# Kernel tuning notes

Hardware: AMD Instinct MI355X
Metric: run time of the kernel (lower is better)

The kernel has to match this reference:

```python
import jax, jax.numpy as jnp
import numpy as np

N, DIN, DOUT = 8192, 256, 128
NEG_SLOPE = 0.01         # F.leaky_relu default
MASK_VAL = -9.0e15       # from the torch source


def setup_inputs() -> dict:
    key = jax.random.key(0)
    kx, kadj, kW, kbW, ka1, ka2, kba = jax.random.split(key, 7)
    x = jax.random.normal(kx, (N, DIN), dtype=jnp.float32)
    adj = jax.random.randint(kadj, (N, N), 0, 2, dtype=jnp.int32)
    # Linear W: input_dim -> output_dim
    W = jax.random.normal(kW, (DIN, DOUT), dtype=jnp.float32) * (1.0 / np.sqrt(DIN))
    bW = jax.random.normal(kbW, (DOUT,), dtype=jnp.float32) * 0.01
    # Linear a: 2*output_dim -> 1, split into the h_i part (a1) and h_j part (a2)
    a1 = jax.random.normal(ka1, (DOUT,), dtype=jnp.float32) * (1.0 / np.sqrt(2 * DOUT))
    a2 = jax.random.normal(ka2, (DOUT,), dtype=jnp.float32) * (1.0 / np.sqrt(2 * DOUT))
    ba = jax.random.normal(kba, (), dtype=jnp.float32) * 0.01
    return {"x": x, "adj": adj, "W": W, "bW": bW, "a1": a1, "a2": a2, "ba": ba}


def reference(x, adj, W, bW, a1, a2, ba):
    # h = W x + b  -> [N, DOUT]
    h = x @ W + bW
    # e[i,j] = leaky_relu(a . [h_i, h_j] + ba) = leaky_relu(a1.h_i + a2.h_j + ba)
    s_src = h @ a1            # [N]
    s_dst = h @ a2            # [N]
    e = s_src[:, None] + s_dst[None, :] + ba   # [N, N]
    e = jnp.where(e > 0, e, NEG_SLOPE * e)
    # mask non-edges, row softmax over neighbors j
    e = jnp.where(adj > 0, e, MASK_VAL)
    alpha = jax.nn.softmax(e, axis=1)          # [N, N]
    # dropout is identity in eval mode (dropout_rate=0)
    return alpha @ h                            # [N, DOUT]
```

## Files before the change

kernel.cpp:

```cpp
#include <hip/hip_runtime.h>
#include <hip/hip_bf16.h>


#define NN 8192
#define DIN 256
#define DOUT 128
#define LOG2E 1.4426950408889634f

typedef __attribute__((ext_vector_type(8))) short short8;
typedef __attribute__((ext_vector_type(4))) float floatx4;
typedef __attribute__((ext_vector_type(4))) unsigned int uintx4;

__global__ void prep_wt(const float* __restrict__ W, __hip_bfloat16* __restrict__ WT) {
    int e = blockIdx.x * blockDim.x + threadIdx.x;
    if (e < DIN * DOUT) {
        int k = e >> 7;
        int d = e & 127;
        WT[d * DIN + k] = __float2bfloat16(W[e]);
    }
}

__global__ __launch_bounds__(256, 4) void gat_h(
    const float* __restrict__ x, const __hip_bfloat16* __restrict__ WT,
    const float* __restrict__ bW, const float* __restrict__ a1, const float* __restrict__ a2,
    __hip_bfloat16* __restrict__ hbB, float* __restrict__ s_src, float* __restrict__ s_dst) {
    int tid = threadIdx.x;
    int w = tid >> 6, lane = tid & 63;
    int lm = lane & 15, lq = lane >> 4;
    int i0 = blockIdx.x * 32;
    int r0 = (w >> 1) * 16;
    int c0 = (w & 1) * 64;

    __shared__ float s1s[32], s2s[32];
    if (tid < 32) { s1s[tid] = 0.f; s2s[tid] = 0.f; }
    __syncthreads();

    floatx4 acc[4] = {};
#pragma unroll
    for (int kk = 0; kk < DIN; kk += 32) {
        const float4* xp = (const float4*)&x[(size_t)(i0 + r0 + lm) * DIN + kk + lq * 8];
        float4 xa = xp[0], xb = xp[1];
        union { short8 v; __hip_bfloat16 h[8]; } af;
        af.h[0] = __float2bfloat16(xa.x); af.h[1] = __float2bfloat16(xa.y);
        af.h[2] = __float2bfloat16(xa.z); af.h[3] = __float2bfloat16(xa.w);
        af.h[4] = __float2bfloat16(xb.x); af.h[5] = __float2bfloat16(xb.y);
        af.h[6] = __float2bfloat16(xb.z); af.h[7] = __float2bfloat16(xb.w);
#pragma unroll
        for (int t = 0; t < 4; t++) {
            int d = c0 + 16 * t + lm;
            short8 bf = *(const short8*)&WT[(size_t)d * DIN + kk + lq * 8];
            acc[t] = __builtin_amdgcn_mfma_f32_16x16x32_bf16(af.v, bf, acc[t], 0, 0, 0);
        }
    }
    float s1[4] = {0.f, 0.f, 0.f, 0.f}, s2[4] = {0.f, 0.f, 0.f, 0.f};
#pragma unroll
    for (int t = 0; t < 4; t++) {
        int d = c0 + 16 * t + lm;
        int f = (c0 >> 4) + t;
        float A1 = a1[d], A2 = a2[d], B = bW[d];
#pragma unroll
        for (int r = 0; r < 4; r++) {
            int k = r0 + lq * 4 + r;
            float h = acc[t][r] + B;
            hbB[(size_t)blockIdx.x * 4096 + f * 512 + (k >> 3) * 128 + lm * 8 + (k & 7)] =
                __float2bfloat16(h);
            s1[r] += h * A1;
            s2[r] += h * A2;
        }
    }
#pragma unroll
    for (int r = 0; r < 4; r++) {
        for (int m = 1; m < 16; m <<= 1) {
            s1[r] += __shfl_xor(s1[r], m, 64);
            s2[r] += __shfl_xor(s2[r], m, 64);
        }
    }
    if (lm == 0) {
#pragma unroll
        for (int r = 0; r < 4; r++) {
            int row = r0 + lq * 4 + r;
            atomicAdd(&s1s[row], s1[r]);
            atomicAdd(&s2s[row], s2[r]);
        }
    }
    __syncthreads();
    if (tid < 32) {
        s_src[i0 + tid] = s1s[tid] * LOG2E;
        s_dst[i0 + tid] = s2s[tid] * LOG2E;
    }
}

__device__ inline short8 make_pfrag(uintx4 m0, uintx4 m1, float ssi, float4 cd0, float4 cd1,
                                    floatx4* accd, const short8 ones) {
    float p[8];
    float e;
    e = ssi + cd0.x; e = fmaxf(e, 0.01f * e); p[0] = m0.x ? __builtin_amdgcn_exp2f(e) : 0.f;
    e = ssi + cd0.y; e = fmaxf(e, 0.01f * e); p[1] = m0.y ? __builtin_amdgcn_exp2f(e) : 0.f;
    e = ssi + cd0.z; e = fmaxf(e, 0.01f * e); p[2] = m0.z ? __builtin_amdgcn_exp2f(e) : 0.f;
    e = ssi + cd0.w; e = fmaxf(e, 0.01f * e); p[3] = m0.w ? __builtin_amdgcn_exp2f(e) : 0.f;
    e = ssi + cd1.x; e = fmaxf(e, 0.01f * e); p[4] = m1.x ? __builtin_amdgcn_exp2f(e) : 0.f;
    e = ssi + cd1.y; e = fmaxf(e, 0.01f * e); p[5] = m1.y ? __builtin_amdgcn_exp2f(e) : 0.f;
    e = ssi + cd1.z; e = fmaxf(e, 0.01f * e); p[6] = m1.z ? __builtin_amdgcn_exp2f(e) : 0.f;
    e = ssi + cd1.w; e = fmaxf(e, 0.01f * e); p[7] = m1.w ? __builtin_amdgcn_exp2f(e) : 0.f;
    union { short8 v; __hip_bfloat162 q[4]; } af;
    af.q[0] = __float22bfloat162_rn(make_float2(p[0], p[1]));
    af.q[1] = __float22bfloat162_rn(make_float2(p[2], p[3]));
    af.q[2] = __float22bfloat162_rn(make_float2(p[4], p[5]));
    af.q[3] = __float22bfloat162_rn(make_float2(p[6], p[7]));
    *accd = __builtin_amdgcn_mfma_f32_16x16x32_bf16(af.v, ones, *accd, 0, 0, 0);
    return af.v;
}

template <int NJT>
__global__ __launch_bounds__(256, 4) void gat_attn(
    const int* __restrict__ adj, const float* __restrict__ s_src,
    const float* __restrict__ s_dst, const float* __restrict__ ba_p,
    const __hip_bfloat16* __restrict__ hbB,
    float* __restrict__ num, float* __restrict__ lpart) {
    int tid = threadIdx.x;
    int w = tid >> 6, lane = tid & 63;
    int lm = lane & 15, lq = lane >> 4;
    int b = blockIdx.x;
    int ib = b & 63;
    int jh = b >> 6;
    int i0 = ib * 128 + w * 32;
    int jb0 = jh * (NJT * 32);

    const int* arow0 = adj + (size_t)(i0 + lm) * NN + jb0 + lq * 8;
    const int* arow1 = arow0 + (size_t)16 * NN;

    float ba = ba_p[0] * LOG2E;
    float ssi0 = s_src[i0 + lm] + ba;
    float ssi1 = s_src[i0 + 16 + lm] + ba;
    const float* sd = s_dst + jb0 + lq * 8;
    const __hip_bfloat16* hb = hbB + ((size_t)(jh * NJT) * 8) * 512 + lane * 8;

    floatx4 acc0[8] = {}, acc1[8] = {};
    floatx4 accd0 = {}, accd1 = {};
    const short8 ones = { 0x3F80, 0x3F80, 0x3F80, 0x3F80, 0x3F80, 0x3F80, 0x3F80, 0x3F80 };

#pragma unroll
    for (int t = 0; t < NJT; t++) {
        const uintx4* a0p = (const uintx4*)(arow0 + t * 32);
        const uintx4* a1p = (const uintx4*)(arow1 + t * 32);
        uintx4 m00 = a0p[0], m01 = a0p[1];
        uintx4 m10 = a1p[0], m11 = a1p[1];
        float4 cd0 = *(const float4*)(sd + t * 32);
        float4 cd1 = *(const float4*)(sd + t * 32 + 4);
        short8 af0 = make_pfrag(m00, m01, ssi0, cd0, cd1, &accd0, ones);
        short8 af1 = make_pfrag(m10, m11, ssi1, cd0, cd1, &accd1, ones);

        const __hip_bfloat16* hbt = hb + (size_t)t * 8 * 512;
#pragma unroll
        for (int f = 0; f < 8; f++) {
            short8 bf = *(const short8*)(hbt + f * 512);
            acc0[f] = __builtin_amdgcn_mfma_f32_16x16x32_bf16(af0, bf, acc0[f], 0, 0, 0);
            acc1[f] = __builtin_amdgcn_mfma_f32_16x16x32_bf16(af1, bf, acc1[f], 0, 0, 0);
        }
    }

    float* nb = num + ((size_t)jh * NN + i0) * DOUT;
#pragma unroll
    for (int f = 0; f < 8; f++)
#pragma unroll
        for (int r = 0; r < 4; r++) {
            __builtin_nontemporal_store(acc0[f][r],
                &nb[(size_t)(lq * 4 + r) * DOUT + f * 16 + lm]);
            __builtin_nontemporal_store(acc1[f][r],
                &nb[(size_t)(16 + lq * 4 + r) * DOUT + f * 16 + lm]);
        }
    if (lm == 0) {
#pragma unroll
        for (int r = 0; r < 4; r++) {
            lpart[(size_t)jh * NN + i0 + lq * 4 + r] = accd0[r];
            lpart[(size_t)jh * NN + i0 + 16 + lq * 4 + r] = accd1[r];
        }
    }
}

__global__ void gat_combine(const float* __restrict__ num, const float* __restrict__ lpart,
                            float* __restrict__ out, int jsplit) {
    int gid = blockIdx.x * blockDim.x + threadIdx.x;
    int idx = gid * 4;
    int i = idx >> 7;
    float den = 0.f;
    for (int s = 0; s < jsplit; s++) den += lpart[(size_t)s * NN + i];
    float inv = 1.0f / den;
    floatx4 o = {0.f, 0.f, 0.f, 0.f};
    for (int s = 0; s < jsplit; s++) {
        floatx4 n = __builtin_nontemporal_load(
            (const floatx4*)&num[(size_t)s * NN * DOUT + idx]);
        o += n;
    }
    o *= inv;
    *(floatx4*)&out[idx] = o;
}

extern "C" void kernel_launch(void* const* d_in, const int* in_sizes, int n_in,
                              void* d_out, int out_size, void* d_ws, size_t ws_size,
                              hipStream_t stream) {
    const float* x  = (const float*)d_in[0];
    const int* adj  = (const int*)d_in[1];
    const float* W  = (const float*)d_in[2];
    const float* bW = (const float*)d_in[3];
    const float* a1 = (const float*)d_in[4];
    const float* a2 = (const float*)d_in[5];
    const float* ba = (const float*)d_in[6];
    float* out = (float*)d_out;

    char* ws = (char*)d_ws;
    __hip_bfloat16* hbB  = (__hip_bfloat16*)ws;
    __hip_bfloat16* WT   = (__hip_bfloat16*)(ws + 2097152);
    float* s_src         = (float*)(ws + 2162688);
    float* s_dst         = (float*)(ws + 2195456);
    float* lpart         = (float*)(ws + 2228224);
    float* num           = (float*)(ws + 2752512);

    int jsplit = (ws_size >= 2752512 + (size_t)16 * NN * DOUT * 4) ? 16 : 8;

    prep_wt<<<128, 256, 0, stream>>>(W, WT);
    gat_h<<<256, 256, 0, stream>>>(x, WT, bW, a1, a2, hbB, s_src, s_dst);
    if (jsplit == 16)
        gat_attn<16><<<1024, 256, 0, stream>>>(adj, s_src, s_dst, ba, hbB, num, lpart);
    else
        gat_attn<32><<<512, 256, 0, stream>>>(adj, s_src, s_dst, ba, hbB, num, lpart);
    gat_combine<<<1024, 256, 0, stream>>>(num, lpart, out, jsplit);
}
```

Measured before the change: 432.7 us.

## Double-buffer adjacency tiles via direct global-to-LDS loads in attention kernel

The adjacency mask loads in the attention loop now go through global_load_lds into a per-wave double-buffered shared-memory region. The next tile is prefetched before the current one is consumed, with explicit vmcnt waits. The goal is to overlap the dominant adj streaming with the exp/MFMA work and to cut register pressure from in-flight loads. In exchange it adds LDS traffic and hand-written waitcnt logic. That logic is fragile because the h-fragment and s_dst global loads also count toward vmcnt.

Result: slower. 458.8 us (+6.0%).

```diff
diff --git a/kernel.cpp b/kernel.cpp
--- a/kernel.cpp
+++ b/kernel.cpp
@@ -126,8 +126,32 @@
     int i0 = ib * 128 + w * 32;
     int jb0 = jh * (NJT * 32);
 
+    __shared__ uintx4 smem[2048];
+
     const int* arow0 = adj + (size_t)(i0 + lm) * NN + jb0 + lq * 8;
     const int* arow1 = arow0 + (size_t)16 * NN;
+
+#define STAGE(tt, par)                                                                      \
+    do {                                                                                    \
+        const int* g0_ = arow0 + (tt) * 32;                                                 \
+        const int* g1_ = arow1 + (tt) * 32;                                                 \
+        __builtin_amdgcn_global_load_lds(                                                   \
+            (const __attribute__((address_space(1))) unsigned int*)g0_,                     \
+            (__attribute__((address_space(3))) unsigned int*)&smem[w * 512 + (par) * 256],  \
+            16, 0, 0);                                                                      \
+        __builtin_amdgcn_global_load_lds(                                                   \
+            (const __attribute__((address_space(1))) unsigned int*)(g0_ + 4),               \
+            (__attribute__((address_space(3))) unsigned int*)&smem[w * 512 + (par) * 256 + 64],  \
+            16, 0, 0);                                                                      \
+        __builtin_amdgcn_global_load_lds(                                                   \
+            (const __attribute__((address_space(1))) unsigned int*)g1_,                     \
+            (__attribute__((address_space(3))) unsigned int*)&smem[w * 512 + (par) * 256 + 128], \
+            16, 0, 0);                                                                      \
+        __builtin_amdgcn_global_load_lds(                                                   \
+            (const __attribute__((address_space(1))) unsigned int*)(g1_ + 4),               \
+            (__attribute__((address_space(3))) unsigned int*)&smem[w * 512 + (par) * 256 + 192], \
+            16, 0, 0);                                                                      \
+    } while (0)
 
     float ba = ba_p[0] * LOG2E;
     float ssi0 = s_src[i0 + lm] + ba;
@@ -139,12 +163,22 @@
     floatx4 accd0 = {}, accd1 = {};
     const short8 ones = { 0x3F80, 0x3F80, 0x3F80, 0x3F80, 0x3F80, 0x3F80, 0x3F80, 0x3F80 };
 
+    STAGE(0, 0);
+
 #pragma unroll
     for (int t = 0; t < NJT; t++) {
-        const uintx4* a0p = (const uintx4*)(arow0 + t * 32);
-        const uintx4* a1p = (const uintx4*)(arow1 + t * 32);
-        uintx4 m00 = a0p[0], m01 = a0p[1];
-        uintx4 m10 = a1p[0], m11 = a1p[1];
+        if (t + 1 < NJT) {
+            STAGE(t + 1, (t + 1) & 1);
+            asm volatile("s_waitcnt vmcnt(4)" ::: "memory");
+        } else {
+            asm volatile("s_waitcnt vmcnt(0)" ::: "memory");
+        }
+        __builtin_amdgcn_sched_barrier(0);
+        int mb = w * 512 + (t & 1) * 256 + lane;
+        uintx4 m00 = smem[mb];
+        uintx4 m01 = smem[mb + 64];
+        uintx4 m10 = smem[mb + 128];
+        uintx4 m11 = smem[mb + 192];
         float4 cd0 = *(const float4*)(sd + t * 32);
         float4 cd1 = *(const float4*)(sd + t * 32 + 4);
         short8 af0 = make_pfrag(m00, m01, ssi0, cd0, cd1, &accd0, ones);
@@ -158,6 +192,7 @@
             acc1[f] = __builtin_amdgcn_mfma_f32_16x16x32_bf16(af1, bf, acc1[f], 0, 0, 0);
         }
     }
+#undef STAGE
 
     float* nb = num + ((size_t)jh * NN + i0) * DOUT;
 #pragma unroll
```
